# Performance work log

Measured on AMD Instinct MI355X. Metric: run time of the kernel, lower is better.

The kernel has to match this reference:

```python
import jax, jax.numpy as jnp
import numpy as np

HID = 128
IN_CH = 271
SEQ = 281
NCLS = 1854
BATCH = 256


def setup_inputs() -> dict:
    key = jax.random.key(0)
    ks = jax.random.split(key, 16)
    s_in = 1.0 / np.sqrt(IN_CH + HID)
    s_h = 1.0 / np.sqrt(HID + HID)
    s_fc = 1.0 / np.sqrt(HID)
    u = lambda k, shape, s: jax.random.uniform(k, shape, jnp.float32, -s, s)
    inp = {
        "X": jax.random.normal(ks[0], (BATCH, IN_CH, SEQ), jnp.float32),
        # layer 0 gates: Linear(in_ch + hid -> hid)
        "Wr0": u(ks[1], (IN_CH + HID, HID), s_in), "br0": u(ks[2], (HID,), s_in),
        "Wu0": u(ks[3], (IN_CH + HID, HID), s_in), "bu0": u(ks[4], (HID,), s_in),
        "Wo0": u(ks[5], (IN_CH + HID, HID), s_in), "bo0": u(ks[6], (HID,), s_in),
        # layer 1 gates: Linear(hid + hid -> hid)
        "Wr1": u(ks[7], (HID + HID, HID), s_h), "br1": u(ks[8], (HID,), s_h),
        "Wu1": u(ks[9], (HID + HID, HID), s_h), "bu1": u(ks[10], (HID,), s_h),
        "Wo1": u(ks[11], (HID + HID, HID), s_h), "bo1": u(ks[12], (HID,), s_h),
        # final classifier
        "Wfc": u(ks[13], (HID, NCLS), s_fc), "bfc": u(ks[14], (NCLS,), s_fc),
    }
    return inp


def _gru_cell(x, h, Wr, br, Wu, bu, Wo, bo):
    combined = jnp.concatenate([x, h], axis=1)            # [B, in+hid]
    reset = jax.nn.sigmoid(combined @ Wr + br)            # [B, hid]
    update = jax.nn.sigmoid(combined @ Wu + bu)
    combined_out = jnp.concatenate([x, reset * h], axis=1)
    out = jnp.tanh(combined_out @ Wo + bo)
    return (1.0 - update) * h + update * out


def reference(X, Wr0, br0, Wu0, bu0, Wo0, bo0,
              Wr1, br1, Wu1, bu1, Wo1, bo1, Wfc, bfc):
    B = X.shape[0]
    Xt = jnp.transpose(X, (2, 0, 1))                      # [T, B, C]
    h0 = jnp.zeros((B, HID), X.dtype)
    h1 = jnp.zeros((B, HID), X.dtype)

    def step(carry, x_t):
        h0, h1 = carry
        h0 = _gru_cell(x_t, h0, Wr0, br0, Wu0, bu0, Wo0, bo0)
        h1 = _gru_cell(h0, h1, Wr1, br1, Wu1, bu1, Wo1, bo1)
        return (h0, h1), None

    (h0, h1), _ = jax.lax.scan(step, (h0, h1), Xt)
    # AdaptiveAvgPool1d(1) over a size-1 dim + rearrange = identity on h1
    # Dropout is identity in eval mode
    return h1 @ Wfc + bfc                                  # [B, num_classes]
```

## Files before the change

### kernel.cpp

```cpp
#include <hip/hip_runtime.h>
#include <math.h>

#define HID    128
#define IN_CH  271
#define SEQ    281
#define NCLS   1854
#define BATCH  256
#define M_TOT  (SEQ * BATCH)
#define KPAD0  288

typedef __attribute__((ext_vector_type(8))) short short8;
typedef __attribute__((ext_vector_type(4))) float floatx4;

#define MFMA16(acc, a, b) acc = __builtin_amdgcn_mfma_f32_16x16x32_bf16((a), (b), (acc), 0, 0, 0)

__device__ __forceinline__ unsigned short f2bf(float f) {
    union { float f; unsigned u; } v; v.f = f;
    unsigned u = v.u;
    u += 0x7FFF + ((u >> 16) & 1);
    return (unsigned short)(u >> 16);
}

__device__ __forceinline__ float fast_rcp(float x) {
    float r;
    asm("v_rcp_f32 %0, %1" : "=v"(r) : "v"(x));
    return r;
}
__device__ __forceinline__ float fast_sigmoid(float s) {
    return fast_rcp(1.f + __expf(-s));
}
__device__ __forceinline__ float fast_tanh(float s) {
    float e = __expf(-2.f * s);
    return __builtin_fmaf(2.f, fast_rcp(1.f + e), -1.f);
}

__device__ __forceinline__ void sync_lds() {
    asm volatile("s_waitcnt lgkmcnt(0)\n\ts_barrier" ::: "memory");
}

__device__ __forceinline__ short8 ldsA_r4(const unsigned short* base, int l15, int kk, int quad) {
    const int row4  = l15 >> 2;
    const int chunk = (4 * kk + quad) ^ (row4 << 1);
    return *(const short8*)(base + row4 * 128 + (chunk << 3));
}
__device__ __forceinline__ int sw_idx4(int row, int c) {
    return row * 128 + ((((c >> 3) ^ (row << 1)) << 3) | (c & 7));
}

__global__ __launch_bounds__(256) void xt_kernel(
    const float* __restrict__ X, unsigned short* __restrict__ Abf)
{
    const int tb = blockIdx.x;
    const int b  = blockIdx.y;
    const int tid = threadIdx.x;
    const int t0 = tb * 64;
    const float* __restrict__ Xb = X + (size_t)b * (IN_CH * SEQ);

    __shared__ float Xl[32][65];

    for (int kc = 0; kc < KPAD0 / 32; ++kc) {
#pragma unroll
        for (int r = 0; r < 8; ++r) {
            int e = tid + 256 * r;
            int kk = e >> 6, tt = e & 63;
            int k = kc * 32 + kk, t = t0 + tt;
            Xl[kk][tt] = (k < IN_CH && t < SEQ) ? Xb[k * SEQ + t] : 0.f;
        }
        __syncthreads();
        {
            int tt = tid >> 2, part = tid & 3;
            int t = t0 + tt;
            if (t < SEQ) {
                union { unsigned short s[8]; uint4 v; } u;
#pragma unroll
                for (int i = 0; i < 8; ++i) u.s[i] = f2bf(Xl[part * 8 + i][tt]);
                *(uint4*)(Abf + ((size_t)b * SEQ + t) * KPAD0 + kc * 32 + part * 8) = u.v;
            }
        }
        __syncthreads();
    }
}

__global__ __launch_bounds__(256) void wt_kernel(
    const float* __restrict__ Wr0, const float* __restrict__ Wu0, const float* __restrict__ Wo0,
    const float* __restrict__ Wr1, const float* __restrict__ Wu1, const float* __restrict__ Wo1,
    unsigned short* __restrict__ Wt0, unsigned short* __restrict__ Wh0,
    unsigned short* __restrict__ Wx1, unsigned short* __restrict__ Wh1)
{
    const int blk  = blockIdx.x;
    const int kind = blk / 3, g = blk % 3;
    const int tid  = threadIdx.x;
    const int n0   = blockIdx.y * 4;

    const float* __restrict__ W =
        (kind <= 1) ? ((g == 0) ? Wr0 : (g == 1) ? Wu0 : Wo0)
                    : ((g == 0) ? Wr1 : (g == 1) ? Wu1 : Wo1);

    if (kind == 0) {
        unsigned short* __restrict__ out = Wt0 + (size_t)g * HID * KPAD0;
        for (int n = n0; n < n0 + 4; ++n)
            for (int k = tid; k < KPAD0; k += 256) {
                float v = (k < IN_CH) ? W[(size_t)k * HID + n] : 0.f;
                out[(size_t)n * KPAD0 + k] = f2bf(v);
            }
    } else {
        const int rbase = (kind == 1) ? IN_CH : (kind == 2) ? 0 : HID;
        unsigned short* __restrict__ out =
            ((kind == 1) ? Wh0 : (kind == 2) ? Wx1 : Wh1) + (size_t)g * HID * HID;
        for (int n = n0; n < n0 + 4; ++n)
            for (int k = tid; k < HID; k += 256)
                out[(size_t)n * HID + k] = f2bf(W[(size_t)(rbase + k) * HID + n]);
    }
}

__global__ __launch_bounds__(256) void gemm_xg(
    const unsigned short* __restrict__ A,
    const unsigned short* __restrict__ Wt,
    const float* __restrict__ br, const float* __restrict__ bu, const float* __restrict__ bo,
    float* __restrict__ XG)
{
    const int g = blockIdx.y;
    const float* __restrict__ bias = (g == 0) ? br : (g == 1) ? bu : bo;
    const unsigned short* __restrict__ B = Wt + (size_t)g * HID * KPAD0;

    __shared__ unsigned short As[128 * 40];
    __shared__ unsigned short Bs[128 * 40];

    const int tid   = threadIdx.x;
    const int lane  = tid & 63;
    const int wave  = tid >> 6;
    const int l15   = lane & 15;
    const int quad  = lane >> 4;
    const int mhalf = wave >> 1;
    const int nhalf = wave & 1;
    const int m0    = blockIdx.x * 128;
    const int tt    = m0 >> 8;
    const int b0m   = m0 & 255;

    floatx4 acc[4][4];
#pragma unroll
    for (int im = 0; im < 4; ++im)
#pragma unroll
        for (int in = 0; in < 4; ++in) acc[im][in] = (floatx4)0.f;

    const int r0 = tid >> 2, p0 = tid & 3;
    const int r1 = (tid + 256) >> 2, p1 = tid & 3;

    for (int kt = 0; kt < KPAD0 / 32; ++kt) {
        if (kt) __syncthreads();
        const int kb = kt * 32;
        uint4 va0 = *(const uint4*)(A + ((size_t)(b0m + r0) * SEQ + tt) * KPAD0 + kb + p0 * 8);
        uint4 va1 = *(const uint4*)(A + ((size_t)(b0m + r1) * SEQ + tt) * KPAD0 + kb + p1 * 8);
        uint4 vb0 = *(const uint4*)(B + (size_t)r0 * KPAD0 + kb + p0 * 8);
        uint4 vb1 = *(const uint4*)(B + (size_t)r1 * KPAD0 + kb + p1 * 8);
        *(uint4*)(As + r0 * 40 + p0 * 8) = va0;
        *(uint4*)(As + r1 * 40 + p1 * 8) = va1;
        *(uint4*)(Bs + r0 * 40 + p0 * 8) = vb0;
        *(uint4*)(Bs + r1 * 40 + p1 * 8) = vb1;
        __syncthreads();

        short8 af[4], bf[4];
#pragma unroll
        for (int im = 0; im < 4; ++im)
            af[im] = *(const short8*)(As + (mhalf * 64 + im * 16 + l15) * 40 + quad * 8);
#pragma unroll
        for (int in = 0; in < 4; ++in)
            bf[in] = *(const short8*)(Bs + (nhalf * 64 + in * 16 + l15) * 40 + quad * 8);
#pragma unroll
        for (int im = 0; im < 4; ++im)
#pragma unroll
            for (int in = 0; in < 4; ++in)
                MFMA16(acc[im][in], af[im], bf[in]);
    }

    float bv[4];
#pragma unroll
    for (int in = 0; in < 4; ++in) bv[in] = bias[nhalf * 64 + in * 16 + l15];
#pragma unroll
    for (int im = 0; im < 4; ++im) {
        const int bb = b0m + mhalf * 64 + im * 16 + quad * 4;
#pragma unroll
        for (int in = 0; in < 4; ++in) {
            const int n = nhalf * 64 + in * 16 + l15;
            float4 v = make_float4(acc[im][in][0] + bv[in], acc[im][in][1] + bv[in],
                                   acc[im][in][2] + bv[in], acc[im][in][3] + bv[in]);
            float* dst = XG + ((size_t)(bb >> 2) * SEQ + tt) * 1536 + ((size_t)g * HID + n) * 4;
            *(float4*)dst = v;
        }
    }
}

__global__ __launch_bounds__(512, 1) void gru_fused(
    const unsigned short* __restrict__ Wh0,
    const unsigned short* __restrict__ Wx1,
    const unsigned short* __restrict__ Wh1,
    const float* __restrict__ XG,
    const float* __restrict__ br1, const float* __restrict__ bu1, const float* __restrict__ bo1,
    float* __restrict__ H1fin)
{
    const int b0   = blockIdx.x * 4;
    const int tid  = threadIdx.x;
    const int w    = tid >> 6;
    const int lane = tid & 63;
    const int l15  = lane & 15;
    const int quad = lane >> 4;
    const int c    = w * 16 + l15;

    __shared__ __attribute__((aligned(16))) unsigned short Hbf0[4 * 128];
    __shared__ __attribute__((aligned(16))) unsigned short Rbf0[4 * 128];
    __shared__ __attribute__((aligned(16))) unsigned short Hbf1[4 * 128];
    __shared__ __attribute__((aligned(16))) unsigned short Rbf1[4 * 128];

    short8 B0r[4], B0u[4], B0o[4], Bxr[4], Bxu[4], Bxo[4], B1r[4], B1u[4], B1o[4];
#pragma unroll
    for (int kk = 0; kk < 4; ++kk) {
        const size_t off = (size_t)c * HID + kk * 32 + quad * 8;
        B0r[kk] = *(const short8*)(Wh0 + off);
        B0u[kk] = *(const short8*)(Wh0 + (size_t)128 * HID + off);
        B0o[kk] = *(const short8*)(Wh0 + (size_t)256 * HID + off);
        Bxr[kk] = *(const short8*)(Wx1 + off);
        Bxu[kk] = *(const short8*)(Wx1 + (size_t)128 * HID + off);
        Bxo[kk] = *(const short8*)(Wx1 + (size_t)256 * HID + off);
        B1r[kk] = *(const short8*)(Wh1 + off);
        B1u[kk] = *(const short8*)(Wh1 + (size_t)128 * HID + off);
        B1o[kk] = *(const short8*)(Wh1 + (size_t)256 * HID + off);
    }

    for (int idx = tid; idx < 4 * 128; idx += 512) {
        Hbf0[idx] = 0; Rbf0[idx] = 0; Hbf1[idx] = 0; Rbf1[idx] = 0;
    }

    float h0s = 0.f, h1s = 0.f, ug0s = 0.f, ug1s = 0.f;

    const float br1c = br1[c], bu1c = bu1[c], bo1c = bo1[c];

    const int swi = sw_idx4(quad, c);

    const float* xgp = XG + (size_t)blockIdx.x * SEQ * 1536 + (size_t)c * 4 + quad;
    float xr = xgp[0];
    float xu = xgp[512];
    float xo = xgp[1024];
    xgp += 1536;
    __syncthreads();

    for (int i = 0; i <= SEQ; ++i) {
        const bool l0 = (i < SEQ);
        const bool l1 = (i > 0);

        float nr, nu, no;
        const bool pf = (i + 1 < SEQ);
        if (pf) {
            nr = xgp[0];
            nu = xgp[512];
            no = xgp[1024];
            xgp += 1536;
        }

        short8 a0[4], a1[4];
#pragma unroll
        for (int kk = 0; kk < 4; ++kk) {
            a0[kk] = ldsA_r4(Hbf0, l15, kk, quad);
            a1[kk] = ldsA_r4(Hbf1, l15, kk, quad);
        }
        floatx4 ar = (floatx4)0.f, au = (floatx4)0.f;
        floatx4 a1r = (floatx4)0.f, a1u = (floatx4)0.f, axo = (floatx4)0.f;
        if (l0) {
#pragma unroll
            for (int kk = 0; kk < 4; ++kk) {
                MFMA16(ar, a0[kk], B0r[kk]);
                MFMA16(au, a0[kk], B0u[kk]);
            }
        }
        if (l1) {
#pragma unroll
            for (int kk = 0; kk < 4; ++kk) {
                MFMA16(a1r, a0[kk], Bxr[kk]);
                MFMA16(a1u, a0[kk], Bxu[kk]);
                MFMA16(axo, a0[kk], Bxo[kk]);
                MFMA16(a1r, a1[kk], B1r[kk]);
                MFMA16(a1u, a1[kk], B1u[kk]);
            }
        }
        if (l0) {
            float rg = fast_sigmoid(ar[0] + xr);
            ug0s = fast_sigmoid(au[0] + xu);
            Rbf0[swi] = f2bf(rg * h0s);
        }
        if (l1) {
            float rg1 = fast_sigmoid(a1r[0] + br1c);
            ug1s = fast_sigmoid(a1u[0] + bu1c);
            Rbf1[swi] = f2bf(rg1 * h1s);
        }
        sync_lds();

        floatx4 ao = (floatx4)0.f;
        if (l0) {
#pragma unroll
            for (int kk = 0; kk < 4; ++kk)
                MFMA16(ao, ldsA_r4(Rbf0, l15, kk, quad), B0o[kk]);
        }
        if (l1) {
#pragma unroll
            for (int kk = 0; kk < 4; ++kk)
                MFMA16(axo, ldsA_r4(Rbf1, l15, kk, quad), B1o[kk]);
        }
        if (l0) {
            float og = fast_tanh(ao[0] + xo);
            h0s = h0s + ug0s * (og - h0s);
            Hbf0[swi] = f2bf(h0s);
        }
        if (l1) {
            float og1 = fast_tanh(axo[0] + bo1c);
            h1s = h1s + ug1s * (og1 - h1s);
            Hbf1[swi] = f2bf(h1s);
        }
        if (pf) { xr = nr; xu = nu; xo = no; }
        sync_lds();
    }

    H1fin[(size_t)(b0 + quad) * HID + c] = h1s;
}

__global__ __launch_bounds__(256) void cls_kernel(
    const float* __restrict__ H1, const float* __restrict__ Wfc,
    const float* __restrict__ bfc, float* __restrict__ out)
{
    const int b = blockIdx.x;
    const int tid = threadIdx.x;
    __shared__ float h[HID];
    if (tid < HID) h[tid] = H1[(size_t)b * HID + tid];
    __syncthreads();
    for (int c = tid; c < NCLS; c += 256) {
        float a = bfc[c];
#pragma unroll 8
        for (int k = 0; k < HID; ++k)
            a += h[k] * Wfc[(size_t)k * NCLS + c];
        out[(size_t)b * NCLS + c] = a;
    }
}

extern "C" void kernel_launch(void* const* d_in, const int* in_sizes, int n_in,
                              void* d_out, int out_size, void* d_ws, size_t ws_size,
                              hipStream_t stream)
{
    const float* X   = (const float*)d_in[0];
    const float* Wr0 = (const float*)d_in[1];
    const float* br0 = (const float*)d_in[2];
    const float* Wu0 = (const float*)d_in[3];
    const float* bu0 = (const float*)d_in[4];
    const float* Wo0 = (const float*)d_in[5];
    const float* bo0 = (const float*)d_in[6];
    const float* Wr1 = (const float*)d_in[7];
    const float* br1 = (const float*)d_in[8];
    const float* Wu1 = (const float*)d_in[9];
    const float* bu1 = (const float*)d_in[10];
    const float* Wo1 = (const float*)d_in[11];
    const float* bo1 = (const float*)d_in[12];
    const float* Wfc = (const float*)d_in[13];
    const float* bfc = (const float*)d_in[14];
    float* out = (float*)d_out;

    char* ws = (char*)d_ws;
    float*          XG    = (float*)ws;
    unsigned short* Abf   = (unsigned short*)(ws + (size_t)M_TOT * 384 * 4);
    float*          H1fin = (float*)Abf;
    unsigned short* Wt0   = (unsigned short*)(ws + (size_t)M_TOT * 384 * 4 + (size_t)M_TOT * KPAD0 * 2);
    unsigned short* Wh0   = Wt0 + (size_t)3 * HID * KPAD0;
    unsigned short* Wx1   = Wh0 + (size_t)384 * HID;
    unsigned short* Wh1   = Wx1 + (size_t)384 * HID;

    wt_kernel<<<dim3(12, 32), 256, 0, stream>>>(Wr0, Wu0, Wo0, Wr1, Wu1, Wo1,
                                                Wt0, Wh0, Wx1, Wh1);
    xt_kernel<<<dim3(5, BATCH), 256, 0, stream>>>(X, Abf);
    gemm_xg  <<<dim3(M_TOT / 128, 3), 256, 0, stream>>>(Abf, Wt0, br0, bu0, bo0, XG);
    gru_fused<<<dim3(64), 512, 0, stream>>>(Wh0, Wx1, Wh1, XG, br1, bu1, bo1, H1fin);
    cls_kernel<<<dim3(BATCH), 256, 0, stream>>>(H1fin, Wfc, bfc, out);
}
```

Before: 525.0 us.

## Fuse transpose, input GEMM and GRU recurrence into one producer-consumer persistent kernel

Merges the X transpose, the layer-0 input-projection GEMM and the recurrent GRU kernel into a single launch. In it, 192 producer blocks build bf16 inputs and XG per time step, and 64 consumer blocks run the recurrence. The two sides synchronise through agent-scope atomic counters, with counters kept in the output buffer. The aim is to overlap the preprocessing GEMM with the serial recurrence and to drop two launches. It also replaces the software bf16 rounding with the hardware v_cvt_pk_bf16_f32 instruction. The change relies on all 256 blocks being co-resident to avoid deadlock, and adds polling overhead in the time-step loop.

```diff
diff --git a/kernel.cpp b/kernel.cpp
--- a/kernel.cpp
+++ b/kernel.cpp
@@ -8,6 +8,9 @@
 #define BATCH  256
 #define M_TOT  (SEQ * BATCH)
 #define KPAD0  288
+#define NPROD  192
+#define XT_UNITS   1280
+#define GEMM_UNITS 843
 
 typedef __attribute__((ext_vector_type(8))) short short8;
 typedef __attribute__((ext_vector_type(4))) float floatx4;
@@ -20,7 +23,11 @@
     u += 0x7FFF + ((u >> 16) & 1);
     return (unsigned short)(u >> 16);
 }
-
+__device__ __forceinline__ unsigned short cvt_bf16(float f) {
+    unsigned r;
+    asm("v_cvt_pk_bf16_f32 %0, %1, %1" : "=v"(r) : "v"(f));
+    return (unsigned short)r;
+}
 __device__ __forceinline__ float fast_rcp(float x) {
     float r;
     asm("v_rcp_f32 %0, %1" : "=v"(r) : "v"(x));
@@ -33,9 +40,16 @@
     float e = __expf(-2.f * s);
     return __builtin_fmaf(2.f, fast_rcp(1.f + e), -1.f);
 }
-
 __device__ __forceinline__ void sync_lds() {
     asm volatile("s_waitcnt lgkmcnt(0)\n\ts_barrier" ::: "memory");
+}
+
+__device__ __forceinline__ void wait_ge(int* p, int tgt) {
+    while (__hip_atomic_load(p, __ATOMIC_ACQUIRE, __HIP_MEMORY_SCOPE_AGENT) < tgt)
+        __builtin_amdgcn_s_sleep(8);
+}
+__device__ __forceinline__ void release_add(int* p, int v) {
+    __hip_atomic_fetch_add(p, v, __ATOMIC_RELEASE, __HIP_MEMORY_SCOPE_AGENT);
 }
 
 __device__ __forceinline__ short8 ldsA_r4(const unsigned short* base, int l15, int kk, int quad) {
@@ -47,50 +61,20 @@
     return row * 128 + ((((c >> 3) ^ (row << 1)) << 3) | (c & 7));
 }
 
-__global__ __launch_bounds__(256) void xt_kernel(
-    const float* __restrict__ X, unsigned short* __restrict__ Abf)
-{
-    const int tb = blockIdx.x;
-    const int b  = blockIdx.y;
-    const int tid = threadIdx.x;
-    const int t0 = tb * 64;
-    const float* __restrict__ Xb = X + (size_t)b * (IN_CH * SEQ);
-
-    __shared__ float Xl[32][65];
-
-    for (int kc = 0; kc < KPAD0 / 32; ++kc) {
-#pragma unroll
-        for (int r = 0; r < 8; ++r) {
-            int e = tid + 256 * r;
-            int kk = e >> 6, tt = e & 63;
-            int k = kc * 32 + kk, t = t0 + tt;
-            Xl[kk][tt] = (k < IN_CH && t < SEQ) ? Xb[k * SEQ + t] : 0.f;
-        }
-        __syncthreads();
-        {
-            int tt = tid >> 2, part = tid & 3;
-            int t = t0 + tt;
-            if (t < SEQ) {
-                union { unsigned short s[8]; uint4 v; } u;
-#pragma unroll
-                for (int i = 0; i < 8; ++i) u.s[i] = f2bf(Xl[part * 8 + i][tt]);
-                *(uint4*)(Abf + ((size_t)b * SEQ + t) * KPAD0 + kc * 32 + part * 8) = u.v;
-            }
-        }
-        __syncthreads();
-    }
-}
-
 __global__ __launch_bounds__(256) void wt_kernel(
     const float* __restrict__ Wr0, const float* __restrict__ Wu0, const float* __restrict__ Wo0,
     const float* __restrict__ Wr1, const float* __restrict__ Wu1, const float* __restrict__ Wo1,
     unsigned short* __restrict__ Wt0, unsigned short* __restrict__ Wh0,
-    unsigned short* __restrict__ Wx1, unsigned short* __restrict__ Wh1)
+    unsigned short* __restrict__ Wx1, unsigned short* __restrict__ Wh1,
+    int* __restrict__ cnt)
 {
     const int blk  = blockIdx.x;
     const int kind = blk / 3, g = blk % 3;
     const int tid  = threadIdx.x;
     const int n0   = blockIdx.y * 4;
+
+    if (blk == 0 && blockIdx.y == 0)
+        for (int j = tid; j < 5 + SEQ; j += 256) cnt[j] = 0;
 
     const float* __restrict__ W =
         (kind <= 1) ? ((g == 0) ? Wr0 : (g == 1) ? Wu0 : Wo0)
@@ -113,212 +97,268 @@
     }
 }
 
-__global__ __launch_bounds__(256) void gemm_xg(
-    const unsigned short* __restrict__ A,
-    const unsigned short* __restrict__ Wt,
-    const float* __restrict__ br, const float* __restrict__ bu, const float* __restrict__ bo,
-    float* __restrict__ XG)
-{
-    const int g = blockIdx.y;
-    const float* __restrict__ bias = (g == 0) ? br : (g == 1) ? bu : bo;
-    const unsigned short* __restrict__ B = Wt + (size_t)g * HID * KPAD0;
-
-    __shared__ unsigned short As[128 * 40];
-    __shared__ unsigned short Bs[128 * 40];
-
-    const int tid   = threadIdx.x;
-    const int lane  = tid & 63;
-    const int wave  = tid >> 6;
-    const int l15   = lane & 15;
-    const int quad  = lane >> 4;
-    const int mhalf = wave >> 1;
-    const int nhalf = wave & 1;
-    const int m0    = blockIdx.x * 128;
-    const int tt    = m0 >> 8;
-    const int b0m   = m0 & 255;
-
-    floatx4 acc[4][4];
-#pragma unroll
-    for (int im = 0; im < 4; ++im)
-#pragma unroll
-        for (int in = 0; in < 4; ++in) acc[im][in] = (floatx4)0.f;
-
-    const int r0 = tid >> 2, p0 = tid & 3;
-    const int r1 = (tid + 256) >> 2, p1 = tid & 3;
-
-    for (int kt = 0; kt < KPAD0 / 32; ++kt) {
-        if (kt) __syncthreads();
-        const int kb = kt * 32;
-        uint4 va0 = *(const uint4*)(A + ((size_t)(b0m + r0) * SEQ + tt) * KPAD0 + kb + p0 * 8);
-        uint4 va1 = *(const uint4*)(A + ((size_t)(b0m + r1) * SEQ + tt) * KPAD0 + kb + p1 * 8);
-        uint4 vb0 = *(const uint4*)(B + (size_t)r0 * KPAD0 + kb + p0 * 8);
-        uint4 vb1 = *(const uint4*)(B + (size_t)r1 * KPAD0 + kb + p1 * 8);
-        *(uint4*)(As + r0 * 40 + p0 * 8) = va0;
-        *(uint4*)(As + r1 * 40 + p1 * 8) = va1;
-        *(uint4*)(Bs + r0 * 40 + p0 * 8) = vb0;
-        *(uint4*)(Bs + r1 * 40 + p1 * 8) = vb1;
-        __syncthreads();
-
-        short8 af[4], bf[4];
-#pragma unroll
-        for (int im = 0; im < 4; ++im)
-            af[im] = *(const short8*)(As + (mhalf * 64 + im * 16 + l15) * 40 + quad * 8);
-#pragma unroll
-        for (int in = 0; in < 4; ++in)
-            bf[in] = *(const short8*)(Bs + (nhalf * 64 + in * 16 + l15) * 40 + quad * 8);
-#pragma unroll
-        for (int im = 0; im < 4; ++im)
-#pragma unroll
-            for (int in = 0; in < 4; ++in)
-                MFMA16(acc[im][in], af[im], bf[in]);
-    }
-
-    float bv[4];
-#pragma unroll
-    for (int in = 0; in < 4; ++in) bv[in] = bias[nhalf * 64 + in * 16 + l15];
-#pragma unroll
-    for (int im = 0; im < 4; ++im) {
-        const int bb = b0m + mhalf * 64 + im * 16 + quad * 4;
-#pragma unroll
-        for (int in = 0; in < 4; ++in) {
-            const int n = nhalf * 64 + in * 16 + l15;
-            float4 v = make_float4(acc[im][in][0] + bv[in], acc[im][in][1] + bv[in],
-                                   acc[im][in][2] + bv[in], acc[im][in][3] + bv[in]);
-            float* dst = XG + ((size_t)(bb >> 2) * SEQ + tt) * 1536 + ((size_t)g * HID + n) * 4;
-            *(float4*)dst = v;
-        }
-    }
-}
-
-__global__ __launch_bounds__(512, 1) void gru_fused(
+__global__ __launch_bounds__(512, 2) void fused_all(
+    const float* __restrict__ X,
+    unsigned short* __restrict__ Abf,
+    const unsigned short* __restrict__ Wt0,
+    const float* __restrict__ br0, const float* __restrict__ bu0, const float* __restrict__ bo0,
+    float* __restrict__ XG,
     const unsigned short* __restrict__ Wh0,
     const unsigned short* __restrict__ Wx1,
     const unsigned short* __restrict__ Wh1,
-    const float* __restrict__ XG,
     const float* __restrict__ br1, const float* __restrict__ bu1, const float* __restrict__ bo1,
-    float* __restrict__ H1fin)
+    float* __restrict__ H1fin,
+    int* __restrict__ cnt)
 {
-    const int b0   = blockIdx.x * 4;
-    const int tid  = threadIdx.x;
-    const int w    = tid >> 6;
-    const int lane = tid & 63;
-    const int l15  = lane & 15;
-    const int quad = lane >> 4;
-    const int c    = w * 16 + l15;
-
-    __shared__ __attribute__((aligned(16))) unsigned short Hbf0[4 * 128];
-    __shared__ __attribute__((aligned(16))) unsigned short Rbf0[4 * 128];
-    __shared__ __attribute__((aligned(16))) unsigned short Hbf1[4 * 128];
-    __shared__ __attribute__((aligned(16))) unsigned short Rbf1[4 * 128];
-
-    short8 B0r[4], B0u[4], B0o[4], Bxr[4], Bxu[4], Bxo[4], B1r[4], B1u[4], B1o[4];
-#pragma unroll
-    for (int kk = 0; kk < 4; ++kk) {
-        const size_t off = (size_t)c * HID + kk * 32 + quad * 8;
-        B0r[kk] = *(const short8*)(Wh0 + off);
-        B0u[kk] = *(const short8*)(Wh0 + (size_t)128 * HID + off);
-        B0o[kk] = *(const short8*)(Wh0 + (size_t)256 * HID + off);
-        Bxr[kk] = *(const short8*)(Wx1 + off);
-        Bxu[kk] = *(const short8*)(Wx1 + (size_t)128 * HID + off);
-        Bxo[kk] = *(const short8*)(Wx1 + (size_t)256 * HID + off);
-        B1r[kk] = *(const short8*)(Wh1 + off);
-        B1u[kk] = *(const short8*)(Wh1 + (size_t)128 * HID + off);
-        B1o[kk] = *(const short8*)(Wh1 + (size_t)256 * HID + off);
+    __shared__ __attribute__((aligned(16))) char smem[40960];
+    __shared__ int rdy_t;
+    const int bid = blockIdx.x;
+    const int tid = threadIdx.x;
+
+    if (bid < NPROD) {
+        const int pid = bid;
+
+        auto xt_unit = [&](int u) {
+            const int tb = u >> 8, b = u & 255;
+            const int t0 = tb * 64;
+            const float* Xb = X + (size_t)b * (IN_CH * SEQ);
+            float (*Xl)[65] = (float (*)[65])smem;
+            for (int kc = 0; kc < KPAD0 / 32; ++kc) {
+#pragma unroll
+                for (int r = 0; r < 4; ++r) {
+                    int e = tid + 512 * r;
+                    int kk = e >> 6, tt = e & 63;
+                    int k = kc * 32 + kk, t = t0 + tt;
+                    Xl[kk][tt] = (k < IN_CH && t < SEQ) ? Xb[k * SEQ + t] : 0.f;
+                }
+                __syncthreads();
+                if (tid < 256) {
+                    int tt = tid >> 2, part = tid & 3, t = t0 + tt;
+                    if (t < SEQ) {
+                        union { unsigned short s[8]; uint4 v; } uu;
+#pragma unroll
+                        for (int i2 = 0; i2 < 8; ++i2) uu.s[i2] = f2bf(Xl[part * 8 + i2][tt]);
+                        *(uint4*)(Abf + ((size_t)b * SEQ + t) * KPAD0 + kc * 32 + part * 8) = uu.v;
+                    }
+                }
+                __syncthreads();
+            }
+            if (tid == 0) release_add(&cnt[tb], 1);
+        };
+
+        const int half = tid >> 8, t2 = tid & 255;
+        unsigned short* As = (unsigned short*)(smem + half * 20480);
+        unsigned short* Bs = As + 5120;
+        const int lane  = t2 & 63;
+        const int wave  = t2 >> 6;
+        const int l15   = lane & 15;
+        const int quad  = lane >> 4;
+        const int mhalf = wave >> 1;
+        const int nhalf = wave & 1;
+        const int r0 = t2 >> 2, p0 = t2 & 3;
+        const int r1 = r0 + 64;
+
+        auto gemm_unit = [&](int p) {
+            const int tt  = p / 3;
+            const int s   = (p % 3) * 2 + half;
+            const int g   = s >> 1;
+            const int b0m = (s & 1) * 128;
+            const unsigned short* Bw = Wt0 + (size_t)g * HID * KPAD0;
+            const float* bias = (g == 0) ? br0 : (g == 1) ? bu0 : bo0;
+
+            wait_ge(&cnt[tt >> 6], 256);
+
+            floatx4 acc[4][4];
+#pragma unroll
+            for (int im = 0; im < 4; ++im)
+#pragma unroll
+                for (int in = 0; in < 4; ++in) acc[im][in] = (floatx4)0.f;
+
+            for (int kt = 0; kt < KPAD0 / 32; ++kt) {
+                __syncthreads();
+                const int kb = kt * 32;
+                uint4 va0 = *(const uint4*)(Abf + ((size_t)(b0m + r0) * SEQ + tt) * KPAD0 + kb + p0 * 8);
+                uint4 va1 = *(const uint4*)(Abf + ((size_t)(b0m + r1) * SEQ + tt) * KPAD0 + kb + p0 * 8);
+                uint4 vb0 = *(const uint4*)(Bw + (size_t)r0 * KPAD0 + kb + p0 * 8);
+                uint4 vb1 = *(const uint4*)(Bw + (size_t)r1 * KPAD0 + kb + p0 * 8);
+                *(uint4*)(As + r0 * 40 + p0 * 8) = va0;
+                *(uint4*)(As + r1 * 40 + p0 * 8) = va1;
+                *(uint4*)(Bs + r0 * 40 + p0 * 8) = vb0;
+                *(uint4*)(Bs + r1 * 40 + p0 * 8) = vb1;
+                __syncthreads();
+
+                short8 bf[4];
+#pragma unroll
+                for (int in = 0; in < 4; ++in)
+                    bf[in] = *(const short8*)(Bs + (nhalf * 64 + in * 16 + l15) * 40 + quad * 8);
+#pragma unroll
+                for (int im = 0; im < 4; ++im) {
+                    short8 af = *(const short8*)(As + (mhalf * 64 + im * 16 + l15) * 40 + quad * 8);
+#pragma unroll
+                    for (int in = 0; in < 4; ++in)
+                        MFMA16(acc[im][in], af, bf[in]);
+                }
+            }
+
+            float bv[4];
+#pragma unroll
+            for (int in = 0; in < 4; ++in) bv[in] = bias[nhalf * 64 + in * 16 + l15];
+#pragma unroll
+            for (int im = 0; im < 4; ++im) {
+                const int bb = b0m + mhalf * 64 + im * 16 + quad * 4;
+#pragma unroll
+                for (int in = 0; in < 4; ++in) {
+                    const int n = nhalf * 64 + in * 16 + l15;
+                    float4 v = make_float4(acc[im][in][0] + bv[in], acc[im][in][1] + bv[in],
+                                           acc[im][in][2] + bv[in], acc[im][in][3] + bv[in]);
+                    float* dst = XG + ((size_t)(bb >> 2) * SEQ + tt) * 1536 + ((size_t)g * HID + n) * 4;
+                    *(float4*)dst = v;
+                }
+            }
+            __syncthreads();
+            if (tid == 0) release_add(&cnt[5 + tt], 2);
+        };
+
+        for (int u = pid; u < 256; u += NPROD)        xt_unit(u);
+        for (int p = pid; p < NPROD; p += NPROD)      gemm_unit(p);
+        for (int u = 256 + pid; u < XT_UNITS; u += NPROD)   xt_unit(u);
+        for (int p = NPROD + pid; p < GEMM_UNITS; p += NPROD) gemm_unit(p);
+
+    } else {
+        const int gb   = bid - NPROD;
+        const int b0   = gb * 4;
+        const int w    = tid >> 6;
+        const int lane = tid & 63;
+        const int l15  = lane & 15;
+        const int quad = lane >> 4;
+        const int c    = w * 16 + l15;
+
+        unsigned short* Hbf0 = (unsigned short*)smem;
+        unsigned short* Rbf0 = Hbf0 + 512;
+        unsigned short* Hbf1 = Hbf0 + 1024;
+        unsigned short* Rbf1 = Hbf0 + 1536;
+        int* cnt5 = cnt + 5;
+
+        short8 B0r[4], B0u[4], B0o[4], Bxr[4], Bxu[4], Bxo[4], B1r[4], B1u[4], B1o[4];
+#pragma unroll
+        for (int kk = 0; kk < 4; ++kk) {
+            const size_t off = (size_t)c * HID + kk * 32 + quad * 8;
+            B0r[kk] = *(const short8*)(Wh0 + off);
+            B0u[kk] = *(const short8*)(Wh0 + (size_t)128 * HID + off);
+            B0o[kk] = *(const short8*)(Wh0 + (size_t)256 * HID + off);
+            Bxr[kk] = *(const short8*)(Wx1 + off);
+            Bxu[kk] = *(const short8*)(Wx1 + (size_t)128 * HID + off);
+            Bxo[kk] = *(const short8*)(Wx1 + (size_t)256 * HID + off);
+            B1r[kk] = *(const short8*)(Wh1 + off);
+            B1u[kk] = *(const short8*)(Wh1 + (size_t)128 * HID + off);
+            B1o[kk] = *(const short8*)(Wh1 + (size_t)256 * HID + off);
+        }
+        Hbf0[tid] = 0; Rbf0[tid] = 0; Hbf1[tid] = 0; Rbf1[tid] = 0;
+
+        float h0s = 0.f, h1s = 0.f, ug0s = 0.f, ug1s = 0.f;
+        const float br1c = br1[c], bu1c = bu1[c], bo1c = bo1[c];
+        const int swi = sw_idx4(quad, c);
+
+        wait_ge(&cnt5[0], 6);
+        wait_ge(&cnt5[1], 6);
+        if (tid == 0) rdy_t = 1;
+
+        const float* xgp = XG + (size_t)gb * SEQ * 1536 + (size_t)c * 4 + quad;
+        float xr = xgp[0];
+        float xu = xgp[512];
+        float xo = xgp[1024];
+        xgp += 1536;
+        __syncthreads();
+
+        for (int i = 0; i <= SEQ; ++i) {
+            const bool l0 = (i < SEQ);
+            const bool l1 = (i > 0);
+            const bool pf = (i + 1 < SEQ);
+            const int  tp = i + 2;
+
+            int pollv = -1;
+            if (tid == 0 && tp < SEQ)
+                pollv = __hip_atomic_load(&cnt5[tp], __ATOMIC_RELAXED, __HIP_MEMORY_SCOPE_AGENT);
+
+            short8 a0[4], a1[4];
+#pragma unroll
+            for (int kk = 0; kk < 4; ++kk) {
+                a0[kk] = ldsA_r4(Hbf0, l15, kk, quad);
+                a1[kk] = ldsA_r4(Hbf1, l15, kk, quad);
+            }
+            floatx4 ar = (floatx4)0.f, au = (floatx4)0.f;
+            floatx4 a1r = (floatx4)0.f, a1u = (floatx4)0.f, axo = (floatx4)0.f;
+            if (l0) {
+#pragma unroll
+                for (int kk = 0; kk < 4; ++kk) {
+                    MFMA16(ar, a0[kk], B0r[kk]);
+                    MFMA16(au, a0[kk], B0u[kk]);
+                }
+            }
+            if (l1) {
+#pragma unroll
+                for (int kk = 0; kk < 4; ++kk) {
+                    MFMA16(a1r, a0[kk], Bxr[kk]);
+                    MFMA16(a1u, a0[kk], Bxu[kk]);
+                    MFMA16(axo, a0[kk], Bxo[kk]);
+                    MFMA16(a1r, a1[kk], B1r[kk]);
+                    MFMA16(a1u, a1[kk], B1u[kk]);
+                }
+            }
+            if (l0) {
+                float rg = fast_sigmoid(ar[0] + xr);
+                ug0s = fast_sigmoid(au[0] + xu);
+                Rbf0[swi] = cvt_bf16(rg * h0s);
+            }
+            if (l1) {
+                float rg1 = fast_sigmoid(a1r[0] + br1c);
+                ug1s = fast_sigmoid(a1u[0] + bu1c);
+                Rbf1[swi] = cvt_bf16(rg1 * h1s);
+            }
+            if (tid == 0 && tp < SEQ && pollv >= 6 && rdy_t == tp - 1) rdy_t = tp;
+            sync_lds();
+
+            float nr = 0.f, nu = 0.f, no = 0.f;
+            if (pf) {
+                if (rdy_t < i + 1) {
+                    wait_ge(&cnt5[i + 1], 6);
+                    if (tid == 0) rdy_t = i + 1;
+                } else {
+                    __builtin_amdgcn_fence(__ATOMIC_ACQUIRE, "agent");
+                }
+                nr = xgp[0];
+                nu = xgp[512];
+                no = xgp[1024];
+                xgp += 1536;
+            }
+
+            floatx4 ao = (floatx4)0.f;
+            if (l0) {
+#pragma unroll
+                for (int kk = 0; kk < 4; ++kk)
+                    MFMA16(ao, ldsA_r4(Rbf0, l15, kk, quad), B0o[kk]);
+            }
+            if (l1) {
+#pragma unroll
+                for (int kk = 0; kk < 4; ++kk)
+                    MFMA16(axo, ldsA_r4(Rbf1, l15, kk, quad), B1o[kk]);
+            }
+            if (l0) {
+                float og = fast_tanh(ao[0] + xo);
+                h0s = h0s + ug0s * (og - h0s);
+                Hbf0[swi] = cvt_bf16(h0s);
+            }
+            if (l1) {
+                float og1 = fast_tanh(axo[0] + bo1c);
+                h1s = h1s + ug1s * (og1 - h1s);
+                Hbf1[swi] = cvt_bf16(h1s);
+            }
+            if (pf) { xr = nr; xu = nu; xo = no; }
+            sync_lds();
+        }
+
+        H1fin[(size_t)(b0 + quad) * HID + c] = h1s;
     }
-
-    for (int idx = tid; idx < 4 * 128; idx += 512) {
-        Hbf0[idx] = 0; Rbf0[idx] = 0; Hbf1[idx] = 0; Rbf1[idx] = 0;
-    }
-
-    float h0s = 0.f, h1s = 0.f, ug0s = 0.f, ug1s = 0.f;
-
-    const float br1c = br1[c], bu1c = bu1[c], bo1c = bo1[c];
-
-    const int swi = sw_idx4(quad, c);
-
-    const float* xgp = XG + (size_t)blockIdx.x * SEQ * 1536 + (size_t)c * 4 + quad;
-    float xr = xgp[0];
-    float xu = xgp[512];
-    float xo = xgp[1024];
-    xgp += 1536;
-    __syncthreads();
-
-    for (int i = 0; i <= SEQ; ++i) {
-        const bool l0 = (i < SEQ);
-        const bool l1 = (i > 0);
-
-        float nr, nu, no;
-        const bool pf = (i + 1 < SEQ);
-        if (pf) {
-            nr = xgp[0];
-            nu = xgp[512];
-            no = xgp[1024];
-            xgp += 1536;
-        }
-
-        short8 a0[4], a1[4];
-#pragma unroll
-        for (int kk = 0; kk < 4; ++kk) {
-            a0[kk] = ldsA_r4(Hbf0, l15, kk, quad);
-            a1[kk] = ldsA_r4(Hbf1, l15, kk, quad);
-        }
-        floatx4 ar = (floatx4)0.f, au = (floatx4)0.f;
-        floatx4 a1r = (floatx4)0.f, a1u = (floatx4)0.f, axo = (floatx4)0.f;
-        if (l0) {
-#pragma unroll
-            for (int kk = 0; kk < 4; ++kk) {
-                MFMA16(ar, a0[kk], B0r[kk]);
-                MFMA16(au, a0[kk], B0u[kk]);
-            }
-        }
-        if (l1) {
-#pragma unroll
-            for (int kk = 0; kk < 4; ++kk) {
-                MFMA16(a1r, a0[kk], Bxr[kk]);
-                MFMA16(a1u, a0[kk], Bxu[kk]);
-                MFMA16(axo, a0[kk], Bxo[kk]);
-                MFMA16(a1r, a1[kk], B1r[kk]);
-                MFMA16(a1u, a1[kk], B1u[kk]);
-            }
-        }
-        if (l0) {
-            float rg = fast_sigmoid(ar[0] + xr);
-            ug0s = fast_sigmoid(au[0] + xu);
-            Rbf0[swi] = f2bf(rg * h0s);
-        }
-        if (l1) {
-            float rg1 = fast_sigmoid(a1r[0] + br1c);
-            ug1s = fast_sigmoid(a1u[0] + bu1c);
-            Rbf1[swi] = f2bf(rg1 * h1s);
-        }
-        sync_lds();
-
-        floatx4 ao = (floatx4)0.f;
-        if (l0) {
-#pragma unroll
-            for (int kk = 0; kk < 4; ++kk)
-                MFMA16(ao, ldsA_r4(Rbf0, l15, kk, quad), B0o[kk]);
-        }
-        if (l1) {
-#pragma unroll
-            for (int kk = 0; kk < 4; ++kk)
-                MFMA16(axo, ldsA_r4(Rbf1, l15, kk, quad), B1o[kk]);
-        }
-        if (l0) {
-            float og = fast_tanh(ao[0] + xo);
-            h0s = h0s + ug0s * (og - h0s);
-            Hbf0[swi] = f2bf(h0s);
-        }
-        if (l1) {
-            float og1 = fast_tanh(axo[0] + bo1c);
-            h1s = h1s + ug1s * (og1 - h1s);
-            Hbf1[swi] = f2bf(h1s);
-        }
-        if (pf) { xr = nr; xu = nu; xo = no; }
-        sync_lds();
-    }
-
-    H1fin[(size_t)(b0 + quad) * HID + c] = h1s;
 }
 
 __global__ __launch_bounds__(256) void cls_kernel(
@@ -368,11 +408,11 @@
     unsigned short* Wh0   = Wt0 + (size_t)3 * HID * KPAD0;
     unsigned short* Wx1   = Wh0 + (size_t)384 * HID;
     unsigned short* Wh1   = Wx1 + (size_t)384 * HID;
+    int*            cnt   = (int*)d_out;
 
     wt_kernel<<<dim3(12, 32), 256, 0, stream>>>(Wr0, Wu0, Wo0, Wr1, Wu1, Wo1,
-                                                Wt0, Wh0, Wx1, Wh1);
-    xt_kernel<<<dim3(5, BATCH), 256, 0, stream>>>(X, Abf);
-    gemm_xg  <<<dim3(M_TOT / 128, 3), 256, 0, stream>>>(Abf, Wt0, br0, bu0, bo0, XG);
-    gru_fused<<<dim3(64), 512, 0, stream>>>(Wh0, Wx1, Wh1, XG, br1, bu1, bo1, H1fin);
+                                                Wt0, Wh0, Wx1, Wh1, cnt);
+    fused_all<<<dim3(256), 512, 0, stream>>>(X, Abf, Wt0, br0, bu0, bo0, XG,
+                                             Wh0, Wx1, Wh1, br1, bu1, bo1, H1fin, cnt);
     cls_kernel<<<dim3(BATCH), 256, 0, stream>>>(H1fin, Wfc, bfc, out);
 }
```

Result: slower. 1.582 ms (+201.3%).

## Fuse X transpose into input-gate GEMM and move bias into recurrence

Applied to the files above, without the earlier changes.

Removes the separate transpose/convert kernel and its bf16 intermediate buffer: the new GEMM reads X directly per batch and time tile, converts it to bf16 in shared memory, and computes all three gates with weights held in registers. XG is re-laid out so each batch element owns a contiguous 384-float gate row, and the gate biases are now added inside the recurrent kernel instead of the GEMM. The recurrent kernel also switches to a hardware bf16 pack instruction for its state conversions. The GEMM now reloads the weight fragments from global memory in every block, and the per-batch grid does less work per block.

```diff
diff --git a/kernel.cpp b/kernel.cpp
--- a/kernel.cpp
+++ b/kernel.cpp
@@ -6,7 +6,6 @@
 #define SEQ    281
 #define NCLS   1854
 #define BATCH  256
-#define M_TOT  (SEQ * BATCH)
 #define KPAD0  288
 
 typedef __attribute__((ext_vector_type(8))) short short8;
@@ -20,7 +19,11 @@
     u += 0x7FFF + ((u >> 16) & 1);
     return (unsigned short)(u >> 16);
 }
-
+__device__ __forceinline__ unsigned short cvt_bf16(float f) {
+    unsigned r;
+    asm("v_cvt_pk_bf16_f32 %0, %1, %1" : "=v"(r) : "v"(f));
+    return (unsigned short)r;
+}
 __device__ __forceinline__ float fast_rcp(float x) {
     float r;
     asm("v_rcp_f32 %0, %1" : "=v"(r) : "v"(x));
@@ -33,7 +36,6 @@
     float e = __expf(-2.f * s);
     return __builtin_fmaf(2.f, fast_rcp(1.f + e), -1.f);
 }
-
 __device__ __forceinline__ void sync_lds() {
     asm volatile("s_waitcnt lgkmcnt(0)\n\ts_barrier" ::: "memory");
 }
@@ -45,40 +47,6 @@
 }
 __device__ __forceinline__ int sw_idx4(int row, int c) {
     return row * 128 + ((((c >> 3) ^ (row << 1)) << 3) | (c & 7));
-}
-
-__global__ __launch_bounds__(256) void xt_kernel(
-    const float* __restrict__ X, unsigned short* __restrict__ Abf)
-{
-    const int tb = blockIdx.x;
-    const int b  = blockIdx.y;
-    const int tid = threadIdx.x;
-    const int t0 = tb * 64;
-    const float* __restrict__ Xb = X + (size_t)b * (IN_CH * SEQ);
-
-    __shared__ float Xl[32][65];
-
-    for (int kc = 0; kc < KPAD0 / 32; ++kc) {
-#pragma unroll
-        for (int r = 0; r < 8; ++r) {
-            int e = tid + 256 * r;
-            int kk = e >> 6, tt = e & 63;
-            int k = kc * 32 + kk, t = t0 + tt;
-            Xl[kk][tt] = (k < IN_CH && t < SEQ) ? Xb[k * SEQ + t] : 0.f;
-        }
-        __syncthreads();
-        {
-            int tt = tid >> 2, part = tid & 3;
-            int t = t0 + tt;
-            if (t < SEQ) {
-                union { unsigned short s[8]; uint4 v; } u;
-#pragma unroll
-                for (int i = 0; i < 8; ++i) u.s[i] = f2bf(Xl[part * 8 + i][tt]);
-                *(uint4*)(Abf + ((size_t)b * SEQ + t) * KPAD0 + kc * 32 + part * 8) = u.v;
-            }
-        }
-        __syncthreads();
-    }
 }
 
 __global__ __launch_bounds__(256) void wt_kernel(
@@ -113,79 +81,86 @@
     }
 }
 
-__global__ __launch_bounds__(256) void gemm_xg(
-    const unsigned short* __restrict__ A,
-    const unsigned short* __restrict__ Wt,
-    const float* __restrict__ br, const float* __restrict__ bu, const float* __restrict__ bo,
+__global__ __launch_bounds__(256) void gemm_bx(
+    const float* __restrict__ X,
+    const unsigned short* __restrict__ Wt0,
     float* __restrict__ XG)
 {
-    const int g = blockIdx.y;
-    const float* __restrict__ bias = (g == 0) ? br : (g == 1) ? bu : bo;
-    const unsigned short* __restrict__ B = Wt + (size_t)g * HID * KPAD0;
-
-    __shared__ unsigned short As[128 * 40];
-    __shared__ unsigned short Bs[128 * 40];
-
-    const int tid   = threadIdx.x;
+    const int b   = blockIdx.x;
+    const int t0  = blockIdx.y * 64;
+    const int tid = threadIdx.x;
+
+    __shared__ float Xl[32][65];
+    __shared__ unsigned short Bt[64 * 40];
+
     const int lane  = tid & 63;
     const int wave  = tid >> 6;
     const int l15   = lane & 15;
     const int quad  = lane >> 4;
     const int mhalf = wave >> 1;
     const int nhalf = wave & 1;
-    const int m0    = blockIdx.x * 128;
-    const int tt    = m0 >> 8;
-    const int b0m   = m0 & 255;
-
-    floatx4 acc[4][4];
-#pragma unroll
-    for (int im = 0; im < 4; ++im)
-#pragma unroll
-        for (int in = 0; in < 4; ++in) acc[im][in] = (floatx4)0.f;
-
-    const int r0 = tid >> 2, p0 = tid & 3;
-    const int r1 = (tid + 256) >> 2, p1 = tid & 3;
-
-    for (int kt = 0; kt < KPAD0 / 32; ++kt) {
-        if (kt) __syncthreads();
+
+    const float* __restrict__ Xb = X + (size_t)b * (IN_CH * SEQ);
+
+    floatx4 acc[12][2];
+#pragma unroll
+    for (int it = 0; it < 12; ++it) {
+        acc[it][0] = (floatx4)0.f;
+        acc[it][1] = (floatx4)0.f;
+    }
+
+    const int tt_s = tid >> 2, part = tid & 3;
+
+    for (int kt = 0; kt < 9; ++kt) {
         const int kb = kt * 32;
-        uint4 va0 = *(const uint4*)(A + ((size_t)(b0m + r0) * SEQ + tt) * KPAD0 + kb + p0 * 8);
-        uint4 va1 = *(const uint4*)(A + ((size_t)(b0m + r1) * SEQ + tt) * KPAD0 + kb + p1 * 8);
-        uint4 vb0 = *(const uint4*)(B + (size_t)r0 * KPAD0 + kb + p0 * 8);
-        uint4 vb1 = *(const uint4*)(B + (size_t)r1 * KPAD0 + kb + p1 * 8);
-        *(uint4*)(As + r0 * 40 + p0 * 8) = va0;
-        *(uint4*)(As + r1 * 40 + p1 * 8) = va1;
-        *(uint4*)(Bs + r0 * 40 + p0 * 8) = vb0;
-        *(uint4*)(Bs + r1 * 40 + p1 * 8) = vb1;
+
+        short8 af[12];
+#pragma unroll
+        for (int it = 0; it < 12; ++it) {
+            const int n = mhalf * 192 + it * 16 + l15;
+            af[it] = *(const short8*)(Wt0 + (size_t)n * KPAD0 + kb + quad * 8);
+        }
+
+#pragma unroll
+        for (int r = 0; r < 8; ++r) {
+            int e = tid + 256 * r;
+            int kk = e >> 6, tt = e & 63;
+            int k = kb + kk, t = t0 + tt;
+            Xl[kk][tt] = (k < IN_CH && t < SEQ) ? Xb[k * SEQ + t] : 0.f;
+        }
         __syncthreads();
 
-        short8 af[4], bf[4];
-#pragma unroll
-        for (int im = 0; im < 4; ++im)
-            af[im] = *(const short8*)(As + (mhalf * 64 + im * 16 + l15) * 40 + quad * 8);
-#pragma unroll
-        for (int in = 0; in < 4; ++in)
-            bf[in] = *(const short8*)(Bs + (nhalf * 64 + in * 16 + l15) * 40 + quad * 8);
-#pragma unroll
-        for (int im = 0; im < 4; ++im)
-#pragma unroll
-            for (int in = 0; in < 4; ++in)
-                MFMA16(acc[im][in], af[im], bf[in]);
-    }
-
-    float bv[4];
-#pragma unroll
-    for (int in = 0; in < 4; ++in) bv[in] = bias[nhalf * 64 + in * 16 + l15];
-#pragma unroll
-    for (int im = 0; im < 4; ++im) {
-        const int bb = b0m + mhalf * 64 + im * 16 + quad * 4;
-#pragma unroll
-        for (int in = 0; in < 4; ++in) {
-            const int n = nhalf * 64 + in * 16 + l15;
-            float4 v = make_float4(acc[im][in][0] + bv[in], acc[im][in][1] + bv[in],
-                                   acc[im][in][2] + bv[in], acc[im][in][3] + bv[in]);
-            float* dst = XG + ((size_t)(bb >> 2) * SEQ + tt) * 1536 + ((size_t)g * HID + n) * 4;
-            *(float4*)dst = v;
+        {
+            union { unsigned short s[8]; uint4 v; } u;
+#pragma unroll
+            for (int i2 = 0; i2 < 8; ++i2) u.s[i2] = f2bf(Xl[part * 8 + i2][tt_s]);
+            *(uint4*)(Bt + tt_s * 40 + part * 8) = u.v;
+        }
+        __syncthreads();
+
+        short8 bf[2];
+#pragma unroll
+        for (int jt = 0; jt < 2; ++jt)
+            bf[jt] = *(const short8*)(Bt + (nhalf * 32 + jt * 16 + l15) * 40 + quad * 8);
+#pragma unroll
+        for (int it = 0; it < 12; ++it) {
+#pragma unroll
+            for (int jt = 0; jt < 2; ++jt)
+                MFMA16(acc[it][jt], af[it], bf[jt]);
+        }
+    }
+
+    const size_t bg_base = ((size_t)(b >> 2) * SEQ) * 1536 + (size_t)(b & 3) * 384;
+#pragma unroll
+    for (int jt = 0; jt < 2; ++jt) {
+        const int t = t0 + nhalf * 32 + jt * 16 + l15;
+        if (t < SEQ) {
+            const size_t trow = bg_base + (size_t)t * 1536;
+#pragma unroll
+            for (int it = 0; it < 12; ++it) {
+                const int n = mhalf * 192 + it * 16 + quad * 4;
+                *(float4*)(XG + trow + n) = *(float4*)&acc[it][jt];
+            }
         }
     }
 }
@@ -195,6 +170,7 @@
     const unsigned short* __restrict__ Wx1,
     const unsigned short* __restrict__ Wh1,
     const float* __restrict__ XG,
+    const float* __restrict__ br0, const float* __restrict__ bu0, const float* __restrict__ bo0,
     const float* __restrict__ br1, const float* __restrict__ bu1, const float* __restrict__ bo1,
     float* __restrict__ H1fin)
 {
@@ -232,14 +208,15 @@
 
     float h0s = 0.f, h1s = 0.f, ug0s = 0.f, ug1s = 0.f;
 
+    const float b0r_c = br0[c], b0u_c = bu0[c], b0o_c = bo0[c];
     const float br1c = br1[c], bu1c = bu1[c], bo1c = bo1[c];
 
     const int swi = sw_idx4(quad, c);
 
-    const float* xgp = XG + (size_t)blockIdx.x * SEQ * 1536 + (size_t)c * 4 + quad;
+    const float* xgp = XG + (size_t)blockIdx.x * SEQ * 1536 + quad * 384 + c;
     float xr = xgp[0];
-    float xu = xgp[512];
-    float xo = xgp[1024];
+    float xu = xgp[128];
+    float xo = xgp[256];
     xgp += 1536;
     __syncthreads();
 
@@ -251,8 +228,8 @@
         const bool pf = (i + 1 < SEQ);
         if (pf) {
             nr = xgp[0];
-            nu = xgp[512];
-            no = xgp[1024];
+            nu = xgp[128];
+            no = xgp[256];
             xgp += 1536;
         }
 
@@ -282,14 +259,14 @@
             }
         }
         if (l0) {
-            float rg = fast_sigmoid(ar[0] + xr);
-            ug0s = fast_sigmoid(au[0] + xu);
-            Rbf0[swi] = f2bf(rg * h0s);
+            float rg = fast_sigmoid(ar[0] + xr + b0r_c);
+            ug0s = fast_sigmoid(au[0] + xu + b0u_c);
+            Rbf0[swi] = cvt_bf16(rg * h0s);
         }
         if (l1) {
             float rg1 = fast_sigmoid(a1r[0] + br1c);
             ug1s = fast_sigmoid(a1u[0] + bu1c);
-            Rbf1[swi] = f2bf(rg1 * h1s);
+            Rbf1[swi] = cvt_bf16(rg1 * h1s);
         }
         sync_lds();
 
@@ -305,14 +282,14 @@
                 MFMA16(axo, ldsA_r4(Rbf1, l15, kk, quad), B1o[kk]);
         }
         if (l0) {
-            float og = fast_tanh(ao[0] + xo);
+            float og = fast_tanh(ao[0] + xo + b0o_c);
             h0s = h0s + ug0s * (og - h0s);
-            Hbf0[swi] = f2bf(h0s);
+            Hbf0[swi] = cvt_bf16(h0s);
         }
         if (l1) {
             float og1 = fast_tanh(axo[0] + bo1c);
             h1s = h1s + ug1s * (og1 - h1s);
-            Hbf1[swi] = f2bf(h1s);
+            Hbf1[swi] = cvt_bf16(h1s);
         }
         if (pf) { xr = nr; xu = nu; xo = no; }
         sync_lds();
@@ -362,17 +339,16 @@
 
     char* ws = (char*)d_ws;
     float*          XG    = (float*)ws;
-    unsigned short* Abf   = (unsigned short*)(ws + (size_t)M_TOT * 384 * 4);
-    float*          H1fin = (float*)Abf;
-    unsigned short* Wt0   = (unsigned short*)(ws + (size_t)M_TOT * 384 * 4 + (size_t)M_TOT * KPAD0 * 2);
+    float*          H1fin = (float*)(ws + (size_t)SEQ * 64 * 1536 * 4);
+    unsigned short* Wt0   = (unsigned short*)(ws + (size_t)SEQ * 64 * 1536 * 4 + (size_t)BATCH * HID * 4);
     unsigned short* Wh0   = Wt0 + (size_t)3 * HID * KPAD0;
     unsigned short* Wx1   = Wh0 + (size_t)384 * HID;
     unsigned short* Wh1   = Wx1 + (size_t)384 * HID;
 
     wt_kernel<<<dim3(12, 32), 256, 0, stream>>>(Wr0, Wu0, Wo0, Wr1, Wu1, Wo1,
                                                 Wt0, Wh0, Wx1, Wh1);
-    xt_kernel<<<dim3(5, BATCH), 256, 0, stream>>>(X, Abf);
-    gemm_xg  <<<dim3(M_TOT / 128, 3), 256, 0, stream>>>(Abf, Wt0, br0, bu0, bo0, XG);
-    gru_fused<<<dim3(64), 512, 0, stream>>>(Wh0, Wx1, Wh1, XG, br1, bu1, bo1, H1fin);
+    gemm_bx  <<<dim3(BATCH, 5), 256, 0, stream>>>(X, Wt0, XG);
+    gru_fused<<<dim3(64), 512, 0, stream>>>(Wh0, Wx1, Wh1, XG,
+                                            br0, bu0, bo0, br1, bu1, bo1, H1fin);
     cls_kernel<<<dim3(BATCH), 256, 0, stream>>>(H1fin, Wfc, bfc, out);
 }
```

Measured after the change: 572.8 us. 1.09x slower.
